# Kernel tuning notes

Measured on AMD Instinct MI355X. Metric: run time of the kernel, lower is better.

## Reference

```python
import jax, jax.numpy as jnp
import numpy as np

BN_EPS = 1e-5
CURVE_LENGTH = 8

def _gumbel_st(logits):
    # straight-through gumbel-softmax (no gumbel noise, temperature=1), over last dim
    y = jax.nn.softmax(logits, axis=-1)
    ind = jnp.argmax(y, axis=-1)
    y_hard = jax.nn.one_hot(ind, logits.shape[-1], dtype=y.dtype)
    return jax.lax.stop_gradient(y_hard - y) + y

def _crossover(cur_vec, nb):
    # cur_vec: (B, c), nb: (B, c, k) -> clamp(1 + cosine, 0, 1), detached
    cur_vec = jax.lax.stop_gradient(cur_vec)
    nb = jax.lax.stop_gradient(nb)
    dot = jnp.einsum('bc,bck->bk', cur_vec, nb)
    n1 = jnp.linalg.norm(cur_vec, axis=1, keepdims=True)        # (B, 1)
    n2 = jnp.linalg.norm(nb, axis=1)                            # (B, k)
    cos = dot / jnp.maximum(n1 * n2, 1e-8)
    return jnp.clip(1.0 + cos, 0.0, 1.0)

def walk_forward(x, adj, cur, agent_w, agent_gamma, agent_beta, agent_mean, agent_var,
                 mom_w, mom_gamma, mom_beta, mom_mean, mom_var):
    bn, c, tot = x.shape
    k = adj.shape[-1]
    cn = cur.shape[1]
    flatten_x = jnp.transpose(x, (0, 2, 1)).reshape(bn * tot, c)
    offset = (jnp.arange(bn, dtype=adj.dtype) * tot)[:, None, None]
    tmp_adj = (adj + offset).reshape(bn * tot, k)
    flatten_cur = (cur + offset).reshape(-1)                    # (bn*cn,)
    inv_agent = agent_gamma / jnp.sqrt(agent_var + BN_EPS)      # (1,)
    inv_mom = mom_gamma / jnp.sqrt(mom_var + BN_EPS)            # (2,)
    rows = jnp.arange(bn * cn)
    curves = []
    pre_feature = cur_feature = cur_feature_cos = pre_feature_cos = None
    for step in range(CURVE_LENGTH):
        if step == 0:
            pre_feature = jnp.transpose(flatten_x[flatten_cur].reshape(bn, cn, c, 1), (0, 2, 1, 3))  # (bn,c,cn,1)
        else:
            cat1 = jnp.concatenate([cur_feature[..., 0], pre_feature[..., 0]], axis=1)  # (bn,2c,cn)
            mlog = jnp.einsum('bcn,oc->bon', cat1, mom_w)
            mlog = (mlog - mom_mean[None, :, None]) * inv_mom[None, :, None] + mom_beta[None, :, None]
            att = jax.nn.softmax(mlog, axis=1).reshape(bn, 1, cn, 2)  # faithful to torch .view
            cat2 = jnp.concatenate([cur_feature, pre_feature], axis=-1)  # (bn,c,cn,2)
            pre_feature = jnp.sum(cat2 * att, axis=-1, keepdims=True)    # (bn,c,cn,1)
            pre_feature_cos = jnp.transpose(pre_feature, (0, 2, 1, 3)).reshape(bn * cn, c)
        pick_idx = tmp_adj[flatten_cur]                                  # (bn*cn, k)
        pv_flat = flatten_x[pick_idx.reshape(-1)].reshape(bn * cn, k, c)
        pv_cos = jnp.transpose(pv_flat, (0, 2, 1))                       # (bn*cn, c, k)
        pick_values = jnp.transpose(pv_flat.reshape(bn, cn, k, c), (0, 3, 1, 2))  # (bn,c,cn,k)
        cat3 = jnp.concatenate([pick_values, jnp.broadcast_to(pre_feature, pick_values.shape)], axis=1)  # (bn,2c,cn,k)
        logits = jnp.einsum('bcnk,c->bnk', cat3, agent_w)[:, None]       # conv2d 1x1 -> (bn,1,cn,k)
        logits = (logits - agent_mean[0]) * inv_agent[0] + agent_beta[0]
        if step != 0:
            d = _crossover(cur_feature_cos - pre_feature_cos, pv_cos - cur_feature_cos[..., None])
            logits = logits * d.reshape(bn, cn, k)[:, None]
        sel = _gumbel_st(logits)                                         # (bn,1,cn,k)
        cur_feature = jnp.sum(pick_values * sel, axis=-1, keepdims=True)  # (bn,c,cn,1)
        cur_feature_cos = jnp.transpose(cur_feature, (0, 2, 1, 3)).reshape(bn * cn, c)
        cur_idx = jnp.argmax(sel, axis=-1).reshape(-1)                   # (bn*cn,)
        flatten_cur = pick_idx[rows, cur_idx]
        curves.append(cur_feature)
    return jnp.concatenate(curves, axis=-1)  # (bn, c, cn, curve_length)

def setup_inputs() -> dict:
    key = jax.random.key(0)
    ks = jax.random.split(key, 12)
    bn, c, tot, k, cn = 16, 64, 8192, 20, 512
    xyz = jax.random.normal(ks[0], (bn, 3, tot), dtype=jnp.float32)
    x = jax.random.normal(ks[1], (bn, c, tot), dtype=jnp.float32)
    adj = jax.random.randint(ks[2], (bn, tot, k), 0, tot)
    cur = jax.random.randint(ks[3], (bn, cn, 1), 0, tot)
    sc = 1.0 / np.sqrt(2 * c)
    agent_w = jax.random.normal(ks[4], (2 * c,), dtype=jnp.float32) * sc
    mom_w = jax.random.normal(ks[5], (2, 2 * c), dtype=jnp.float32) * sc
    agent_gamma = 1.0 + 0.1 * jax.random.normal(ks[6], (1,), dtype=jnp.float32)
    agent_beta = 0.1 * jax.random.normal(ks[7], (1,), dtype=jnp.float32)
    agent_mean = 0.1 * jax.random.normal(ks[8], (1,), dtype=jnp.float32)
    agent_var = jax.random.uniform(ks[9], (1,), minval=0.5, maxval=1.5, dtype=jnp.float32)
    mom_gamma = 1.0 + 0.1 * jax.random.normal(ks[10], (2,), dtype=jnp.float32)
    mom_beta = 0.1 * jax.random.normal(ks[11], (2,), dtype=jnp.float32)
    mom_mean = 0.1 * jax.random.normal(jax.random.fold_in(key, 101), (2,), dtype=jnp.float32)
    mom_var = jax.random.uniform(jax.random.fold_in(key, 102), (2,), minval=0.5, maxval=1.5, dtype=jnp.float32)
    return {"xyz": xyz, "x": x, "adj": adj, "cur": cur,
            "agent_w": agent_w, "agent_gamma": agent_gamma, "agent_beta": agent_beta,
            "agent_mean": agent_mean, "agent_var": agent_var,
            "mom_w": mom_w, "mom_gamma": mom_gamma, "mom_beta": mom_beta,
            "mom_mean": mom_mean, "mom_var": mom_var}

def reference(xyz, x, adj, cur, agent_w, agent_gamma, agent_beta, agent_mean, agent_var,
              mom_w, mom_gamma, mom_beta, mom_mean, mom_var):
    # xyz is accepted (as in the torch forward) but never used: the original code
    # calls `xyz.transpose(1, 2).contiguous` without invoking it.
    return walk_forward(x, adj, cur, agent_w, agent_gamma, agent_beta, agent_mean,
                        agent_var, mom_w, mom_gamma, mom_beta, mom_mean, mom_var)
```

## Files before the change

kernel.cpp:

```cpp
#include <hip/hip_runtime.h>
#include <cmath>

#define BN 16
#define CDIM 64
#define TOT 8192
#define KNB 20
#define CN 512
#define NSTEPS 8
#define WPB 16
#define BPB 32
#define WSTRIDE 577
#define LINE 32
#define MAGIC 0x5A17ECE1u
#define POISON 0xAAAAAAAAu

typedef float vf4 __attribute__((ext_vector_type(4)));
typedef unsigned uv4 __attribute__((ext_vector_type(4)));

__device__ __forceinline__ float dot4(float a, float b, float c, float d,
                                      float wa, float wb, float wc, float wd) {
  return a * wa + b * wb + c * wc + d * wd;
}

template <int CTRL>
__device__ __forceinline__ float dpp_add(float v) {
  int o = __builtin_amdgcn_update_dpp(0, __float_as_int(v), CTRL, 0xF, 0xF, true);
  return v + __int_as_float(o);
}

__device__ __forceinline__ float gred16(float v) {
  v = dpp_add<0xB1>(v);
  v = dpp_add<0x4E>(v);
  v = dpp_add<0x141>(v);
  v = dpp_add<0x140>(v);
  return v;
}

__device__ __forceinline__ const vf4* vptr(const float* base, unsigned boff) {
  return (const vf4*)((const char*)base + boff);
}
__device__ __forceinline__ float ldf(const float* base, unsigned boff) {
  return *(const float*)((const char*)base + boff);
}

__global__ __launch_bounds__(256, 2) void walk_kernel(
    const float* __restrict__ x, const int* __restrict__ adj, const int* __restrict__ cur,
    const float* __restrict__ agent_w, const float* __restrict__ agent_gamma,
    const float* __restrict__ agent_beta, const float* __restrict__ agent_mean,
    const float* __restrict__ agent_var, const float* __restrict__ mom_w,
    const float* __restrict__ mom_gamma, const float* __restrict__ mom_beta,
    const float* __restrict__ mom_mean, const float* __restrict__ mom_var,
    float* __restrict__ xt, float* __restrict__ pa,
    float* __restrict__ out, float* __restrict__ sbuf,
    unsigned int* __restrict__ pflag) {
  __shared__ float lds_out[WPB * WSTRIDE];
  const int tid  = threadIdx.x;
  const int lane = tid & 63;
  const int wv   = tid >> 6;
  const int g    = lane >> 4;
  const int L    = lane & 15;
  const int b     = (blockIdx.x & 7) + (((blockIdx.x >> 8) & 1) << 3);
  const int chunk = (blockIdx.x >> 3) & 31;
  const int w     = wv * 4 + g;
  const int n     = chunk * WPB + w;
  const int c0    = L << 2;
  const int mbase = (n << 2) & 1023;
  const int moff  = (chunk >= 16) ? 1 : 0;

  {
    float (*tile)[65] = (float (*)[65])lds_out;
    const vf4 awp = *(const vf4*)(agent_w + (L << 2));
#pragma unroll 1
    for (int i = 0; i < 4; ++i) {
      const int t0 = ((chunk << 2) + i) << 6;
#pragma unroll
      for (int k = 0; k < 4; ++k) {
        int fid = tid + k * 256;
        int cc = fid >> 4, qt = (fid & 15) << 2;
        float4 vv = *(const float4*)(x + ((size_t)b * CDIM + cc) * TOT + t0 + qt);
        tile[cc][qt + 0] = vv.x; tile[cc][qt + 1] = vv.y;
        tile[cc][qt + 2] = vv.z; tile[cc][qt + 3] = vv.w;
      }
      __syncthreads();
#pragma unroll
      for (int k = 0; k < 4; ++k) {
        int fid = tid + k * 256;
        int tt = fid >> 4, qc = (fid & 15) << 2;
        vf4 vv = {tile[qc + 0][tt], tile[qc + 1][tt], tile[qc + 2][tt], tile[qc + 3][tt]};
        float* dst = xt + ((size_t)b * TOT + t0 + tt) * CDIM + qc;
        asm volatile("global_store_dwordx4 %0, %1, off sc0 sc1" :: "v"(dst), "v"(vv) : "memory");
        float part = gred16(dot4(vv.x, vv.y, vv.z, vv.w, awp.x, awp.y, awp.z, awp.w));
        if ((tid & 15) == 0)
          __hip_atomic_store(pa + (size_t)b * TOT + t0 + tt, part,
                             __ATOMIC_RELAXED, __HIP_MEMORY_SCOPE_AGENT);
      }
      __syncthreads();
    }
    asm volatile("s_waitcnt vmcnt(0)" ::: "memory");
    __builtin_amdgcn_s_barrier();
    if (tid == 0)
      __hip_atomic_store(pflag + ((size_t)b * BPB + chunk) * LINE, MAGIC,
                         __ATOMIC_RELAXED, __HIP_MEMORY_SCOPE_AGENT);
    if (tid < BPB) {
      const unsigned int* f = pflag + ((size_t)b * BPB + tid) * LINE;
      while (__hip_atomic_load(f, __ATOMIC_RELAXED, __HIP_MEMORY_SCOPE_AGENT) != MAGIC)
        __builtin_amdgcn_s_sleep(2);
    }
    __builtin_amdgcn_s_barrier();
    asm volatile("" ::: "memory");
  }

  const vf4 aw2  = *(const vf4*)(agent_w + 64 + c0);
  const vf4 mw0a = *(const vf4*)(mom_w + c0);
  const vf4 mw0b = *(const vf4*)(mom_w + 64 + c0);
  const vf4 mw1a = *(const vf4*)(mom_w + 128 + c0);
  const vf4 mw1b = *(const vf4*)(mom_w + 192 + c0);
  const float amean  = agent_mean[0];
  const float abeta  = agent_beta[0];
  const float ainv   = agent_gamma[0] / sqrtf(agent_var[0] + 1e-5f);
  const float m0mean = mom_mean[0], m1mean = mom_mean[1];
  const float m0inv  = mom_gamma[0] / sqrtf(mom_var[0] + 1e-5f);
  const float m1inv  = mom_gamma[1] / sqrtf(mom_var[1] + 1e-5f);
  const float m0beta = mom_beta[0], m1beta = mom_beta[1];

  const float* xb   = xt + (size_t)b * TOT * CDIM;
  const float* pab  = pa + (size_t)b * TOT;
  const int*   adjb = adj + (size_t)b * TOT * KNB;
  float*       lout = lds_out + w * WSTRIDE;

  int t = cur[b * CN + n];
  vf4 pf = *vptr(xb, ((unsigned)t << 8) + (unsigned)(c0 << 2));
  vf4 cf = pf;
  vf4 u  = (vf4){0.f, 0.f, 0.f, 0.f};
  float A0v = 0.f, A1v = 0.f;

  int   idx[KNB];
  vf4   nv[KNB];
  float pav[KNB];
  float sq[KNB];
  {
    const int4* arow = (const int4*)((const char*)adjb + (unsigned)t * 80u);
    int4 q0 = arow[0], q1 = arow[1], q2 = arow[2], q3 = arow[3], q4 = arow[4];
    int tmp[KNB] = {q0.x, q0.y, q0.z, q0.w, q1.x, q1.y, q1.z, q1.w,
                    q2.x, q2.y, q2.z, q2.w, q3.x, q3.y, q3.z, q3.w,
                    q4.x, q4.y, q4.z, q4.w};
#pragma unroll
    for (int j = 0; j < KNB; ++j) idx[j] = tmp[j];
#pragma unroll
    for (int j = 0; j < KNB; ++j) {
      nv[j]  = *vptr(xb, ((unsigned)idx[j] << 8) + (unsigned)(c0 << 2));
      pav[j] = ldf(pab, (unsigned)idx[j] << 2) * ainv;
    }
  }

  __builtin_amdgcn_s_setprio(1);
#pragma unroll 1
  for (int s = 0; s < NSTEPS; ++s) {
    float n1 = 0.f;
    if (s > 0) {
      pf.x = A0v * cf.x + A1v * pf.x;
      pf.y = A0v * cf.y + A1v * pf.y;
      pf.z = A0v * cf.z + A1v * pf.z;
      pf.w = A0v * cf.w + A1v * pf.w;
      u.x = cf.x - pf.x; u.y = cf.y - pf.y; u.z = cf.z - pf.z; u.w = cf.w - pf.w;
      n1 = sqrtf(gred16(u.x * u.x + u.y * u.y + u.z * u.z + u.w * u.w));
    }
    float pw = gred16(pf.x * aw2.x + pf.y * aw2.y + pf.z * aw2.z + pf.w * aw2.w);
    float lbase = (pw - amean) * ainv + abeta;

    float bestp = -3.4e38f;
    int   bestt = 0;
    vf4   bestv = (vf4){0.f, 0.f, 0.f, 0.f};
#pragma unroll
    for (int j = 0; j < KNB; ++j) {
      const vf4 v = nv[j];
      float logit = pav[j] + lbase;
      float p;
      if (s > 0) {
        float tx = v.x - cf.x, ty = v.y - cf.y, tz = v.z - cf.z, tw = v.w - cf.w;
        float su = tx * u.x + ty * u.y + tz * u.z + tw * u.w;
        su = gred16(su);
        float den  = fmaxf(n1 * sq[j], 1e-8f);
        float cosv = su * __builtin_amdgcn_rcpf(den);
        float dfac = fminf(fmaxf(1.0f + cosv, 0.0f), 1.0f);
        p = logit * dfac;
      } else {
        p = logit;
      }
      if (p > bestp) { bestp = p; bestt = idx[j]; bestv = v; }
    }
    cf = bestv;
    t  = bestt;
    lout[(c0 + 0) * 9 + s] = cf.x;
    lout[(c0 + 1) * 9 + s] = cf.y;
    lout[(c0 + 2) * 9 + s] = cf.z;
    lout[(c0 + 3) * 9 + s] = cf.w;

    if (s < NSTEPS - 1) {
      float p0 = cf.x * mw0a.x + cf.y * mw0a.y + cf.z * mw0a.z + cf.w * mw0a.w +
                 pf.x * mw0b.x + pf.y * mw0b.y + pf.z * mw0b.z + pf.w * mw0b.w;
      float p1 = cf.x * mw1a.x + cf.y * mw1a.y + cf.z * mw1a.z + cf.w * mw1a.w +
                 pf.x * mw1b.x + pf.y * mw1b.y + pf.z * mw1b.z + pf.w * mw1b.w;
      p0 = gred16(p0);
      p1 = gred16(p1);
      float mlog0 = (p0 - m0mean) * m0inv + m0beta;
      float mlog1 = (p1 - m1mean) * m1inv + m1beta;
      float mx = fmaxf(mlog0, mlog1);
      float e0 = expf(mlog0 - mx), e1 = expf(mlog1 - mx);
      float sinv = 1.0f / (e0 + e1);
      float* sb = sbuf + ((size_t)(b * NSTEPS + s + 1) << 10);
      if (L == 0) {
        unsigned long long pk =
            (unsigned long long)__float_as_uint(e0 * sinv) |
            ((unsigned long long)__float_as_uint(e1 * sinv) << 32);
        __hip_atomic_store((unsigned long long*)sb + n, pk,
                           __ATOMIC_RELAXED, __HIP_MEMORY_SCOPE_AGENT);
      }
      __builtin_amdgcn_s_setprio(0);
      const char* pollp = (const char*)sb + ((unsigned)mbase << 2);
      uv4 pr;
      asm volatile("global_load_dwordx4 %0, %1, off sc0 sc1"
                   : "=v"(pr) : "v"(pollp) : "memory");
      const int4* arow = (const int4*)((const char*)adjb + (unsigned)t * 80u);
      int4 q0 = arow[0], q1 = arow[1], q2 = arow[2], q3 = arow[3], q4 = arow[4];
      int tmp[KNB] = {q0.x, q0.y, q0.z, q0.w, q1.x, q1.y, q1.z, q1.w,
                      q2.x, q2.y, q2.z, q2.w, q3.x, q3.y, q3.z, q3.w,
                      q4.x, q4.y, q4.z, q4.w};
#pragma unroll
      for (int j = 0; j < KNB; ++j) idx[j] = tmp[j];
#pragma unroll
      for (int j = 0; j < KNB; ++j) {
        nv[j]  = *vptr(xb, ((unsigned)idx[j] << 8) + (unsigned)(c0 << 2));
        pav[j] = ldf(pab, (unsigned)idx[j] << 2) * ainv;
      }
#pragma unroll
      for (int j = 0; j < KNB; ++j) {
        const vf4 v = nv[j];
        float tx = v.x - cf.x, ty = v.y - cf.y, tz = v.z - cf.z, tw = v.w - cf.w;
        float sn = tx * tx + ty * ty + tz * tz + tw * tw;
        sq[j] = sqrtf(gred16(sn));
      }
      {
        asm volatile("s_waitcnt vmcnt(0)" ::: "memory");
        unsigned w0 = moff ? pr.y : pr.x;
        unsigned w2 = moff ? pr.w : pr.z;
        while (w0 == POISON || w2 == POISON) {
          __builtin_amdgcn_s_sleep(1);
          asm volatile("global_load_dwordx4 %0, %1, off sc0 sc1"
                       : "=v"(pr) : "v"(pollp) : "memory");
          asm volatile("s_waitcnt vmcnt(0)" ::: "memory");
          w0 = moff ? pr.y : pr.x;
          w2 = moff ? pr.w : pr.z;
        }
        A0v = __uint_as_float(w0);
        A1v = __uint_as_float(w2);
      }
      __builtin_amdgcn_s_setprio(1);
      asm volatile("" ::: "memory");
    }
  }

#pragma unroll
  for (int e = 0; e < 4; ++e) {
    const float* src = lout + (c0 + e) * 9;
    float4 w0 = make_float4(src[0], src[1], src[2], src[3]);
    float4 w1 = make_float4(src[4], src[5], src[6], src[7]);
    float* op = out + (((size_t)(b * CDIM + c0 + e) * CN) + n) * NSTEPS;
    *(float4*)(op)     = w0;
    *(float4*)(op + 4) = w1;
  }
}

extern "C" void kernel_launch(void* const* d_in, const int* in_sizes, int n_in,
                              void* d_out, int out_size, void* d_ws, size_t ws_size,
                              hipStream_t stream) {
  (void)in_sizes; (void)n_in; (void)out_size; (void)ws_size;
  const float* x          = (const float*)d_in[1];
  const int*   adj        = (const int*)d_in[2];
  const int*   cur        = (const int*)d_in[3];
  const float* agent_w    = (const float*)d_in[4];
  const float* agent_gamma= (const float*)d_in[5];
  const float* agent_beta = (const float*)d_in[6];
  const float* agent_mean = (const float*)d_in[7];
  const float* agent_var  = (const float*)d_in[8];
  const float* mom_w      = (const float*)d_in[9];
  const float* mom_gamma  = (const float*)d_in[10];
  const float* mom_beta   = (const float*)d_in[11];
  const float* mom_mean   = (const float*)d_in[12];
  const float* mom_var    = (const float*)d_in[13];
  float* out = (float*)d_out;

  char* ws = (char*)d_ws;
  const size_t xt_bytes   = (size_t)BN * TOT * CDIM * sizeof(float);
  const size_t sbuf_bytes = (size_t)BN * NSTEPS * 2 * CN * sizeof(float);
  const size_t pa_bytes   = (size_t)BN * TOT * sizeof(float);
  float*        xt    = (float*)ws;
  float*        sbuf  = (float*)(ws + xt_bytes);
  float*        pab   = (float*)(ws + xt_bytes + sbuf_bytes);
  unsigned int* pflag = (unsigned int*)(ws + xt_bytes + sbuf_bytes + pa_bytes);

  walk_kernel<<<BN * BPB, 256, 0, stream>>>(x, adj, cur, agent_w, agent_gamma, agent_beta,
                                            agent_mean, agent_var, mom_w, mom_gamma, mom_beta,
                                            mom_mean, mom_var, xt, pab, out, sbuf, pflag);
}
```

Measured before the change: 160.8 us.

## Transpose-reduce neighbor dot products across lanes and use cross-lane argmax

Replaces the 20 separate 16-lane butterfly reductions per step (for cosine dot products and neighbor norms) with a transpose-style reduction, so each lane ends up owning one or two neighbors' full sums. The argmax then runs as a cross-lane DPP/swizzle reduction with index tie-break, and the winning feature vector is picked by select. Per-neighbor arrays idx/pav/sq are replaced with per-lane scalars, which lowers register pressure and the number of shuffle instructions. The poll now uses two relaxed atomic loads instead of an inline-asm dwordx4 load, which may change memory traffic and ordering behavior.

```diff
diff --git a/kernel.cpp b/kernel.cpp
--- a/kernel.cpp
+++ b/kernel.cpp
@@ -15,7 +15,6 @@
 #define POISON 0xAAAAAAAAu
 
 typedef float vf4 __attribute__((ext_vector_type(4)));
-typedef unsigned uv4 __attribute__((ext_vector_type(4)));
 
 __device__ __forceinline__ float dot4(float a, float b, float c, float d,
                                       float wa, float wb, float wc, float wd) {
@@ -26,6 +25,22 @@
 __device__ __forceinline__ float dpp_add(float v) {
   int o = __builtin_amdgcn_update_dpp(0, __float_as_int(v), CTRL, 0xF, 0xF, true);
   return v + __int_as_float(o);
+}
+template <int CTRL>
+__device__ __forceinline__ float dppf(float v) {
+  return __int_as_float(__builtin_amdgcn_update_dpp(0, __float_as_int(v), CTRL, 0xF, 0xF, true));
+}
+template <int CTRL>
+__device__ __forceinline__ int dppi(int v) {
+  return __builtin_amdgcn_update_dpp(0, v, CTRL, 0xF, 0xF, true);
+}
+template <int MASK>
+__device__ __forceinline__ float swzf(float v) {
+  return __int_as_float(__builtin_amdgcn_ds_swizzle(__float_as_int(v), MASK));
+}
+template <int MASK>
+__device__ __forceinline__ int swzi(int v) {
+  return __builtin_amdgcn_ds_swizzle(v, MASK);
 }
 
 __device__ __forceinline__ float gred16(float v) {
@@ -34,6 +49,41 @@
   v = dpp_add<0x141>(v);
   v = dpp_add<0x140>(v);
   return v;
+}
+
+__device__ __forceinline__ float sred16(float* a, bool L0, bool L1, bool L2, bool L3) {
+#pragma unroll
+  for (int i = 0; i < 16; ++i) a[i] = a[i] + dppf<0xB1>(a[i]);
+  float b[8];
+#pragma unroll
+  for (int m = 0; m < 8; ++m) b[m] = L0 ? a[2 * m + 1] : a[2 * m];
+#pragma unroll
+  for (int m = 0; m < 8; ++m) b[m] = b[m] + dppf<0x4E>(b[m]);
+  float c[4];
+#pragma unroll
+  for (int m = 0; m < 4; ++m) c[m] = L1 ? b[2 * m + 1] : b[2 * m];
+#pragma unroll
+  for (int m = 0; m < 4; ++m) c[m] = c[m] + swzf<0x101F>(c[m]);
+  float d[2];
+#pragma unroll
+  for (int m = 0; m < 2; ++m) d[m] = L2 ? c[2 * m + 1] : c[2 * m];
+#pragma unroll
+  for (int m = 0; m < 2; ++m) d[m] = d[m] + swzf<0x201F>(d[m]);
+  return L3 ? d[1] : d[0];
+}
+
+__device__ __forceinline__ float sred4(float* a, bool L0, bool L1) {
+#pragma unroll
+  for (int i = 0; i < 4; ++i) a[i] = a[i] + dppf<0xB1>(a[i]);
+  float b[2];
+  b[0] = L0 ? a[1] : a[0];
+  b[1] = L0 ? a[3] : a[2];
+#pragma unroll
+  for (int m = 0; m < 2; ++m) b[m] = b[m] + dppf<0x4E>(b[m]);
+  float c = L1 ? b[1] : b[0];
+  c = c + swzf<0x101F>(c);
+  c = c + swzf<0x201F>(c);
+  return c;
 }
 
 __device__ __forceinline__ const vf4* vptr(const float* base, unsigned boff) {
@@ -59,6 +109,7 @@
   const int wv   = tid >> 6;
   const int g    = lane >> 4;
   const int L    = lane & 15;
+  const bool L0 = L & 1, L1 = L & 2, L2 = L & 4, L3 = L & 8;
   const int b     = (blockIdx.x & 7) + (((blockIdx.x >> 8) & 1) << 3);
   const int chunk = (blockIdx.x >> 3) & 31;
   const int w     = wv * 4 + g;
@@ -134,10 +185,10 @@
   vf4 u  = (vf4){0.f, 0.f, 0.f, 0.f};
   float A0v = 0.f, A1v = 0.f;
 
-  int   idx[KNB];
   vf4   nv[KNB];
-  float pav[KNB];
-  float sq[KNB];
+  int   tL1, tL2;
+  float pvL1, pvL2;
+  float sqL1 = 0.f, sqL2 = 0.f;
   {
     const int4* arow = (const int4*)((const char*)adjb + (unsigned)t * 80u);
     int4 q0 = arow[0], q1 = arow[1], q2 = arow[2], q3 = arow[3], q4 = arow[4];
@@ -145,12 +196,16 @@
                     q2.x, q2.y, q2.z, q2.w, q3.x, q3.y, q3.z, q3.w,
                     q4.x, q4.y, q4.z, q4.w};
 #pragma unroll
-    for (int j = 0; j < KNB; ++j) idx[j] = tmp[j];
-#pragma unroll
-    for (int j = 0; j < KNB; ++j) {
-      nv[j]  = *vptr(xb, ((unsigned)idx[j] << 8) + (unsigned)(c0 << 2));
-      pav[j] = ldf(pab, (unsigned)idx[j] << 2) * ainv;
-    }
+    for (int j = 0; j < KNB; ++j)
+      nv[j] = *vptr(xb, ((unsigned)tmp[j] << 8) + (unsigned)(c0 << 2));
+    tL1 = tmp[0];
+#pragma unroll
+    for (int j = 1; j < 16; ++j) tL1 = (L == j) ? tmp[j] : tL1;
+    tL2 = tmp[16];
+#pragma unroll
+    for (int q = 1; q < 4; ++q) tL2 = ((L & 3) == q) ? tmp[16 + q] : tL2;
+    pvL1 = ldf(pab, (unsigned)tL1 << 2) * ainv;
+    pvL2 = ldf(pab, (unsigned)tL2 << 2) * ainv;
   }
 
   __builtin_amdgcn_s_setprio(1);
@@ -168,29 +223,70 @@
     float pw = gred16(pf.x * aw2.x + pf.y * aw2.y + pf.z * aw2.z + pf.w * aw2.w);
     float lbase = (pw - amean) * ainv + abeta;
 
-    float bestp = -3.4e38f;
-    int   bestt = 0;
-    vf4   bestv = (vf4){0.f, 0.f, 0.f, 0.f};
-#pragma unroll
-    for (int j = 0; j < KNB; ++j) {
-      const vf4 v = nv[j];
-      float logit = pav[j] + lbase;
-      float p;
-      if (s > 0) {
+    float p1, p2;
+    if (s > 0) {
+      float up[16], up2[4];
+#pragma unroll
+      for (int j = 0; j < 16; ++j) {
+        const vf4 v = nv[j];
         float tx = v.x - cf.x, ty = v.y - cf.y, tz = v.z - cf.z, tw = v.w - cf.w;
-        float su = tx * u.x + ty * u.y + tz * u.z + tw * u.w;
-        su = gred16(su);
-        float den  = fmaxf(n1 * sq[j], 1e-8f);
-        float cosv = su * __builtin_amdgcn_rcpf(den);
-        float dfac = fminf(fmaxf(1.0f + cosv, 0.0f), 1.0f);
-        p = logit * dfac;
-      } else {
-        p = logit;
-      }
-      if (p > bestp) { bestp = p; bestt = idx[j]; bestv = v; }
-    }
-    cf = bestv;
-    t  = bestt;
+        up[j] = tx * u.x + ty * u.y + tz * u.z + tw * u.w;
+      }
+#pragma unroll
+      for (int q = 0; q < 4; ++q) {
+        const vf4 v = nv[16 + q];
+        float tx = v.x - cf.x, ty = v.y - cf.y, tz = v.z - cf.z, tw = v.w - cf.w;
+        up2[q] = tx * u.x + ty * u.y + tz * u.z + tw * u.w;
+      }
+      float su1 = sred16(up, L0, L1, L2, L3);
+      float su2 = sred4(up2, L0, L1);
+      float den1  = fmaxf(n1 * sqL1, 1e-8f);
+      float cos1  = su1 * __builtin_amdgcn_rcpf(den1);
+      float dfac1 = fminf(fmaxf(1.0f + cos1, 0.0f), 1.0f);
+      p1 = (pvL1 + lbase) * dfac1;
+      float den2  = fmaxf(n1 * sqL2, 1e-8f);
+      float cos2  = su2 * __builtin_amdgcn_rcpf(den2);
+      float dfac2 = fminf(fmaxf(1.0f + cos2, 0.0f), 1.0f);
+      p2 = (pvL2 + lbase) * dfac2;
+    } else {
+      p1 = pvL1 + lbase;
+      p2 = pvL2 + lbase;
+    }
+
+    float bp; int bj, bt;
+    {
+      bool tk = p2 > p1;
+      bp = tk ? p2 : p1;
+      bj = tk ? (16 + (L & 3)) : L;
+      bt = tk ? tL2 : tL1;
+    }
+#define AMAX_STAGE(GF, GI)                                        \
+    {                                                             \
+      float po = GF(bp); int jo = GI(bj); int to = GI(bt);        \
+      bool better = (po > bp) || ((po == bp) && (jo < bj));       \
+      bp = better ? po : bp;                                      \
+      bj = better ? jo : bj;                                      \
+      bt = better ? to : bt;                                      \
+    }
+    AMAX_STAGE(dppf<0xB1>, dppi<0xB1>)
+    AMAX_STAGE(dppf<0x4E>, dppi<0x4E>)
+    AMAX_STAGE(swzf<0x101F>, swzi<0x101F>)
+    AMAX_STAGE(swzf<0x201F>, swzi<0x201F>)
+#undef AMAX_STAGE
+
+    {
+      vf4 bv = nv[0];
+#pragma unroll
+      for (int j = 1; j < KNB; ++j) {
+        bool e = (bj == j);
+        bv.x = e ? nv[j].x : bv.x;
+        bv.y = e ? nv[j].y : bv.y;
+        bv.z = e ? nv[j].z : bv.z;
+        bv.w = e ? nv[j].w : bv.w;
+      }
+      cf = bv;
+    }
+    t = bt;
     lout[(c0 + 0) * 9 + s] = cf.x;
     lout[(c0 + 1) * 9 + s] = cf.y;
     lout[(c0 + 2) * 9 + s] = cf.z;
@@ -199,12 +295,12 @@
     if (s < NSTEPS - 1) {
       float p0 = cf.x * mw0a.x + cf.y * mw0a.y + cf.z * mw0a.z + cf.w * mw0a.w +
                  pf.x * mw0b.x + pf.y * mw0b.y + pf.z * mw0b.z + pf.w * mw0b.w;
-      float p1 = cf.x * mw1a.x + cf.y * mw1a.y + cf.z * mw1a.z + cf.w * mw1a.w +
-                 pf.x * mw1b.x + pf.y * mw1b.y + pf.z * mw1b.z + pf.w * mw1b.w;
-      p0 = gred16(p0);
-      p1 = gred16(p1);
+      float p1m = cf.x * mw1a.x + cf.y * mw1a.y + cf.z * mw1a.z + cf.w * mw1a.w +
+                  pf.x * mw1b.x + pf.y * mw1b.y + pf.z * mw1b.z + pf.w * mw1b.w;
+      p0  = gred16(p0);
+      p1m = gred16(p1m);
       float mlog0 = (p0 - m0mean) * m0inv + m0beta;
-      float mlog1 = (p1 - m1mean) * m1inv + m1beta;
+      float mlog1 = (p1m - m1mean) * m1inv + m1beta;
       float mx = fmaxf(mlog0, mlog1);
       float e0 = expf(mlog0 - mx), e1 = expf(mlog1 - mx);
       float sinv = 1.0f / (e0 + e1);
@@ -217,44 +313,50 @@
                            __ATOMIC_RELAXED, __HIP_MEMORY_SCOPE_AGENT);
       }
       __builtin_amdgcn_s_setprio(0);
-      const char* pollp = (const char*)sb + ((unsigned)mbase << 2);
-      uv4 pr;
-      asm volatile("global_load_dwordx4 %0, %1, off sc0 sc1"
-                   : "=v"(pr) : "v"(pollp) : "memory");
+      const unsigned* q0p = (const unsigned*)sb + mbase + moff;
+      const unsigned* q2p = q0p + 2;
+      unsigned w0 = __hip_atomic_load(q0p, __ATOMIC_RELAXED, __HIP_MEMORY_SCOPE_AGENT);
+      unsigned w2 = __hip_atomic_load(q2p, __ATOMIC_RELAXED, __HIP_MEMORY_SCOPE_AGENT);
       const int4* arow = (const int4*)((const char*)adjb + (unsigned)t * 80u);
       int4 q0 = arow[0], q1 = arow[1], q2 = arow[2], q3 = arow[3], q4 = arow[4];
       int tmp[KNB] = {q0.x, q0.y, q0.z, q0.w, q1.x, q1.y, q1.z, q1.w,
                       q2.x, q2.y, q2.z, q2.w, q3.x, q3.y, q3.z, q3.w,
                       q4.x, q4.y, q4.z, q4.w};
 #pragma unroll
-      for (int j = 0; j < KNB; ++j) idx[j] = tmp[j];
-#pragma unroll
-      for (int j = 0; j < KNB; ++j) {
-        nv[j]  = *vptr(xb, ((unsigned)idx[j] << 8) + (unsigned)(c0 << 2));
-        pav[j] = ldf(pab, (unsigned)idx[j] << 2) * ainv;
-      }
-#pragma unroll
-      for (int j = 0; j < KNB; ++j) {
-        const vf4 v = nv[j];
-        float tx = v.x - cf.x, ty = v.y - cf.y, tz = v.z - cf.z, tw = v.w - cf.w;
-        float sn = tx * tx + ty * ty + tz * tz + tw * tw;
-        sq[j] = sqrtf(gred16(sn));
-      }
+      for (int j = 0; j < KNB; ++j)
+        nv[j] = *vptr(xb, ((unsigned)tmp[j] << 8) + (unsigned)(c0 << 2));
+      tL1 = tmp[0];
+#pragma unroll
+      for (int j = 1; j < 16; ++j) tL1 = (L == j) ? tmp[j] : tL1;
+      tL2 = tmp[16];
+#pragma unroll
+      for (int q = 1; q < 4; ++q) tL2 = ((L & 3) == q) ? tmp[16 + q] : tL2;
+      pvL1 = ldf(pab, (unsigned)tL1 << 2) * ainv;
+      pvL2 = ldf(pab, (unsigned)tL2 << 2) * ainv;
       {
-        asm volatile("s_waitcnt vmcnt(0)" ::: "memory");
-        unsigned w0 = moff ? pr.y : pr.x;
-        unsigned w2 = moff ? pr.w : pr.z;
-        while (w0 == POISON || w2 == POISON) {
-          __builtin_amdgcn_s_sleep(1);
-          asm volatile("global_load_dwordx4 %0, %1, off sc0 sc1"
-                       : "=v"(pr) : "v"(pollp) : "memory");
-          asm volatile("s_waitcnt vmcnt(0)" ::: "memory");
-          w0 = moff ? pr.y : pr.x;
-          w2 = moff ? pr.w : pr.z;
+        float sp[16], sp2[4];
+#pragma unroll
+        for (int j = 0; j < 16; ++j) {
+          const vf4 v = nv[j];
+          float tx = v.x - cf.x, ty = v.y - cf.y, tz = v.z - cf.z, tw = v.w - cf.w;
+          sp[j] = tx * tx + ty * ty + tz * tz + tw * tw;
         }
-        A0v = __uint_as_float(w0);
-        A1v = __uint_as_float(w2);
-      }
+#pragma unroll
+        for (int q2i = 0; q2i < 4; ++q2i) {
+          const vf4 v = nv[16 + q2i];
+          float tx = v.x - cf.x, ty = v.y - cf.y, tz = v.z - cf.z, tw = v.w - cf.w;
+          sp2[q2i] = tx * tx + ty * ty + tz * tz + tw * tw;
+        }
+        sqL1 = sqrtf(sred16(sp, L0, L1, L2, L3));
+        sqL2 = sqrtf(sred4(sp2, L0, L1));
+      }
+      while (w0 == POISON || w2 == POISON) {
+        __builtin_amdgcn_s_sleep(1);
+        w0 = __hip_atomic_load(q0p, __ATOMIC_RELAXED, __HIP_MEMORY_SCOPE_AGENT);
+        w2 = __hip_atomic_load(q2p, __ATOMIC_RELAXED, __HIP_MEMORY_SCOPE_AGENT);
+      }
+      A0v = __uint_as_float(w0);
+      A1v = __uint_as_float(w2);
       __builtin_amdgcn_s_setprio(1);
       asm volatile("" ::: "memory");
     }
```

After: 153.6 us. 1.05x faster.
